# Kernel tuning notes

Measured on AMD Instinct MI355X. Metric: run time of the kernel, lower is better.

The kernel has to match this reference:

```python
import jax, jax.numpy as jnp
import numpy as np

B, H, S, D = 8, 8, 2048, 64

def setup_inputs() -> dict:
    key = jax.random.key(0)
    kq, kk, kv = jax.random.split(key, 3)
    queries = jax.random.normal(kq, (B, H, S, D), dtype=jnp.float32)
    keys = jax.random.normal(kk, (B, H, S, D), dtype=jnp.float32)
    values = jax.random.normal(kv, (B, H, S, D), dtype=jnp.float32)
    return {"queries": queries, "keys": keys, "values": values}

def reference(queries, keys, values):
    # scores: [B,H,S,S] = Q K^T / sqrt(D)
    scale = 1.0 / jnp.sqrt(jnp.asarray(queries.shape[-1], dtype=jnp.float32))
    scores = jnp.einsum('bhqd,bhkd->bhqk', queries, keys) * scale
    attn = jax.nn.softmax(scores, axis=-1)
    # dropout is identity at eval (p=0.0)
    return jnp.einsum('bhqk,bhkd->bhqd', attn, values)
```

## Files before the change

### kernel.cpp

```cpp
#include <hip/hip_runtime.h>

#define S_LEN 2048
#define HEAD_D 64
#define NH 64
#define KVB 64
#define NKT (S_LEN / KVB)
#define RS 72
#define KREG (KVB * RS)
#define IMG_USH (2 * KREG)
#define IMG_B (IMG_USH * 2)
#define WS_V5 ((size_t)NH * NKT * IMG_B)
#define IMG4_USH (KVB * HEAD_D * 2)

typedef float f32x4  __attribute__((ext_vector_type(4)));
typedef float f32x16 __attribute__((ext_vector_type(16)));
typedef __bf16 bf16x8 __attribute__((ext_vector_type(8)));

static __device__ __forceinline__ unsigned short f2bf(float x) {
  __bf16 h = (__bf16)x;
  return __builtin_bit_cast(unsigned short, h);
}
static __device__ __forceinline__ void gload_lds16(const void* g, void* l) {
  __builtin_amdgcn_global_load_lds(
      (const __attribute__((address_space(1))) unsigned int*)g,
      (__attribute__((address_space(3))) unsigned int*)l, 16, 0, 0);
}
static __device__ __forceinline__ int vpos(int kv) {
  return (kv & ~15) | (((kv >> 2) & 1) << 3) | (((kv >> 3) & 1) << 2) | (kv & 3);
}

__global__ __launch_bounds__(256) void pack_kv5(
    const float* __restrict__ K, const float* __restrict__ V,
    unsigned short* __restrict__ ws)
{
  const int kt = blockIdx.x;
  const int bh = blockIdx.y;
  const int t  = threadIdx.x;
  const float* Kg = K + ((size_t)bh * S_LEN + (size_t)kt * KVB) * HEAD_D;
  const float* Vg = V + ((size_t)bh * S_LEN + (size_t)kt * KVB) * HEAD_D;
  unsigned short* img = ws + ((size_t)bh * NKT + kt) * IMG_USH;

  __shared__ unsigned short vt[KREG];

#pragma unroll
  for (int i = 0; i < 4; ++i) {
    const int e   = t * 4 + i * 1024;
    const int row = e >> 6;
    const int col = e & 63;
    float4 k4 = *(const float4*)(Kg + e);
    ushort4 kb;
    kb.x = f2bf(k4.x); kb.y = f2bf(k4.y); kb.z = f2bf(k4.z); kb.w = f2bf(k4.w);
    *(ushort4*)&img[row * RS + col] = kb;
    float4 v4 = *(const float4*)(Vg + e);
    const int p = vpos(row);
    vt[(col + 0) * RS + p] = f2bf(v4.x);
    vt[(col + 1) * RS + p] = f2bf(v4.y);
    vt[(col + 2) * RS + p] = f2bf(v4.z);
    vt[(col + 3) * RS + p] = f2bf(v4.w);
  }
  __syncthreads();
  char* dst = (char*)(img + KREG);
  const char* src = (const char*)vt;
#pragma unroll
  for (int i = 0; i < 3; ++i) {
    const int off = t * 16 + i * 4096;
    if (off < 9216) *(uint4*)(dst + off) = *(const uint4*)(src + off);
  }
}

#define QBLK 256
#define NQT (S_LEN / QBLK)
__global__ __launch_bounds__(256, 2) void flash_attn_fwd_v6(
    const float* __restrict__ Q, const unsigned short* __restrict__ ws,
    float* __restrict__ O)
{
  __shared__ unsigned short lds[2][IMG_USH];

  const int tid  = threadIdx.x;
  const int wave = tid >> 6;
  const int lane = tid & 63;
  const int l31  = lane & 31;
  const int hi   = lane >> 5;

  const int bid = blockIdx.x;
  const int swz = (bid & 7) * 64 + (bid >> 3);
  const int bh  = swz >> 3;
  const int qt  = swz & 7;

  const float* Qh = Q + (size_t)bh * (S_LEN * HEAD_D);
  float*       Oh = O + (size_t)bh * (S_LEN * HEAD_D);
  const char*  gbase = (const char*)(ws + (size_t)bh * NKT * IMG_USH);

  const int qrowA = qt * QBLK + wave * 64 + l31;
  const int qrowB = qrowA + 32;

  bf16x8 qfA[4], qfB[4];
#pragma unroll
  for (int c = 0; c < 4; ++c) {
    const float* qa = Qh + (size_t)qrowA * HEAD_D + c * 16 + hi * 8;
    float4 a0 = *(const float4*)qa;
    float4 a1 = *(const float4*)(qa + 4);
    qfA[c][0] = (__bf16)a0.x; qfA[c][1] = (__bf16)a0.y;
    qfA[c][2] = (__bf16)a0.z; qfA[c][3] = (__bf16)a0.w;
    qfA[c][4] = (__bf16)a1.x; qfA[c][5] = (__bf16)a1.y;
    qfA[c][6] = (__bf16)a1.z; qfA[c][7] = (__bf16)a1.w;
    const float* qb = Qh + (size_t)qrowB * HEAD_D + c * 16 + hi * 8;
    float4 b0 = *(const float4*)qb;
    float4 b1 = *(const float4*)(qb + 4);
    qfB[c][0] = (__bf16)b0.x; qfB[c][1] = (__bf16)b0.y;
    qfB[c][2] = (__bf16)b0.z; qfB[c][3] = (__bf16)b0.w;
    qfB[c][4] = (__bf16)b1.x; qfB[c][5] = (__bf16)b1.y;
    qfB[c][6] = (__bf16)b1.z; qfB[c][7] = (__bf16)b1.w;
  }

  f32x16 oaA0, oaA1, oaB0, oaB1;
#pragma unroll
  for (int i = 0; i < 16; ++i) { oaA0[i] = 0.0f; oaA1[i] = 0.0f; oaB0[i] = 0.0f; oaB1[i] = 0.0f; }
  float lA = 0.0f, lB = 0.0f;
  const float K2 = 0.18033688f;
  const float C2 = -23.0831206f;

  auto stage = [&](const char* g, unsigned short* Lp) {
    char* lb = (char*)Lp;
#pragma unroll
    for (int i = 0; i < 5; ++i) {
      const int ch = wave + i * 4;
      if (ch < 18) gload_lds16(g + ch * 1024 + lane * 16, lb + ch * 1024);
    }
  };

  auto compute = [&](const unsigned short* Lp) {
    const char* ka = (const char*)Lp + l31 * 144 + hi * 16;
    f32x16 p0A, p1A, p0B, p1B;
#pragma unroll
    for (int i = 0; i < 16; ++i) { p0A[i] = 0.0f; p1A[i] = 0.0f; p0B[i] = 0.0f; p1B[i] = 0.0f; }
    __builtin_amdgcn_s_setprio(1);
#pragma unroll
    for (int c = 0; c < 4; ++c) {
      bf16x8 kf0 = *(const bf16x8*)(ka + c * 32);
      bf16x8 kf1 = *(const bf16x8*)(ka + 4608 + c * 32);
      p0A = __builtin_amdgcn_mfma_f32_32x32x16_bf16(kf0, qfA[c], p0A, 0, 0, 0);
      p0B = __builtin_amdgcn_mfma_f32_32x32x16_bf16(kf0, qfB[c], p0B, 0, 0, 0);
      p1A = __builtin_amdgcn_mfma_f32_32x32x16_bf16(kf1, qfA[c], p1A, 0, 0, 0);
      p1B = __builtin_amdgcn_mfma_f32_32x32x16_bf16(kf1, qfB[c], p1B, 0, 0, 0);
    }
    __builtin_amdgcn_s_setprio(0);

#pragma unroll
    for (int i = 0; i < 16; ++i) {
      p0A[i] = __builtin_amdgcn_exp2f(__builtin_fmaf(p0A[i], K2, C2));
      p1A[i] = __builtin_amdgcn_exp2f(__builtin_fmaf(p1A[i], K2, C2));
      p0B[i] = __builtin_amdgcn_exp2f(__builtin_fmaf(p0B[i], K2, C2));
      p1B[i] = __builtin_amdgcn_exp2f(__builtin_fmaf(p1B[i], K2, C2));
    }
    float sA[16], sB[16];
#pragma unroll
    for (int i = 0; i < 16; ++i) { sA[i] = p0A[i] + p1A[i]; sB[i] = p0B[i] + p1B[i]; }
#pragma unroll
    for (int st = 8; st >= 1; st >>= 1)
#pragma unroll
      for (int i = 0; i < st; ++i) { sA[i] += sA[i + st]; sB[i] += sB[i + st]; }
    lA += sA[0];
    lB += sB[0];

    __builtin_amdgcn_s_setprio(1);
#pragma unroll
    for (int kc = 0; kc < 4; ++kc) {
      const f32x16& psA = (kc < 2) ? p0A : p1A;
      const f32x16& psB = (kc < 2) ? p0B : p1B;
      const int rb = (kc & 1) * 8;
      unsigned a0, a1, a2, a3, b0, b1, b2, b3;
      asm("v_cvt_pk_bf16_f32 %0, %1, %2" : "=v"(a0) : "v"(psA[rb + 0]), "v"(psA[rb + 1]));
      asm("v_cvt_pk_bf16_f32 %0, %1, %2" : "=v"(a1) : "v"(psA[rb + 2]), "v"(psA[rb + 3]));
      asm("v_cvt_pk_bf16_f32 %0, %1, %2" : "=v"(a2) : "v"(psA[rb + 4]), "v"(psA[rb + 5]));
      asm("v_cvt_pk_bf16_f32 %0, %1, %2" : "=v"(a3) : "v"(psA[rb + 6]), "v"(psA[rb + 7]));
      asm("v_cvt_pk_bf16_f32 %0, %1, %2" : "=v"(b0) : "v"(psB[rb + 0]), "v"(psB[rb + 1]));
      asm("v_cvt_pk_bf16_f32 %0, %1, %2" : "=v"(b1) : "v"(psB[rb + 2]), "v"(psB[rb + 3]));
      asm("v_cvt_pk_bf16_f32 %0, %1, %2" : "=v"(b2) : "v"(psB[rb + 4]), "v"(psB[rb + 5]));
      asm("v_cvt_pk_bf16_f32 %0, %1, %2" : "=v"(b3) : "v"(psB[rb + 6]), "v"(psB[rb + 7]));
      uint4 wa; wa.x = a0; wa.y = a1; wa.z = a2; wa.w = a3;
      uint4 wb; wb.x = b0; wb.y = b1; wb.z = b2; wb.w = b3;
      bf16x8 pfA = __builtin_bit_cast(bf16x8, wa);
      bf16x8 pfB = __builtin_bit_cast(bf16x8, wb);
      bf16x8 vf0 = *(const bf16x8*)(ka + 9216 + kc * 32);
      bf16x8 vf1 = *(const bf16x8*)(ka + 9216 + 4608 + kc * 32);
      oaA0 = __builtin_amdgcn_mfma_f32_32x32x16_bf16(vf0, pfA, oaA0, 0, 0, 0);
      oaB0 = __builtin_amdgcn_mfma_f32_32x32x16_bf16(vf0, pfB, oaB0, 0, 0, 0);
      oaA1 = __builtin_amdgcn_mfma_f32_32x32x16_bf16(vf1, pfA, oaA1, 0, 0, 0);
      oaB1 = __builtin_amdgcn_mfma_f32_32x32x16_bf16(vf1, pfB, oaB1, 0, 0, 0);
    }
    __builtin_amdgcn_s_setprio(0);
  };

  stage(gbase, &lds[0][0]);
  __syncthreads();
  const char* g = gbase + IMG_B;

  for (int kt = 0; kt < NKT; kt += 2) {
    stage(g, &lds[1][0]);
    g += IMG_B;
    compute(&lds[0][0]);
    __syncthreads();
    const char* gs = (kt + 2 < NKT) ? g : gbase;
    stage(gs, &lds[0][0]);
    g += IMG_B;
    compute(&lds[1][0]);
    __syncthreads();
  }

  const float invA = 1.0f / (lA + __shfl_xor(lA, 32));
  const float invB = 1.0f / (lB + __shfl_xor(lB, 32));
  float* orA = Oh + (size_t)qrowA * HEAD_D;
  float* orB = Oh + (size_t)qrowB * HEAD_D;
#pragma unroll
  for (int gg = 0; gg < 4; ++gg) {
    float4 o;
    o.x = oaA0[4 * gg + 0] * invA; o.y = oaA0[4 * gg + 1] * invA;
    o.z = oaA0[4 * gg + 2] * invA; o.w = oaA0[4 * gg + 3] * invA;
    *(float4*)&orA[gg * 8 + hi * 4] = o;
    o.x = oaA1[4 * gg + 0] * invA; o.y = oaA1[4 * gg + 1] * invA;
    o.z = oaA1[4 * gg + 2] * invA; o.w = oaA1[4 * gg + 3] * invA;
    *(float4*)&orA[32 + gg * 8 + hi * 4] = o;
    o.x = oaB0[4 * gg + 0] * invB; o.y = oaB0[4 * gg + 1] * invB;
    o.z = oaB0[4 * gg + 2] * invB; o.w = oaB0[4 * gg + 3] * invB;
    *(float4*)&orB[gg * 8 + hi * 4] = o;
    o.x = oaB1[4 * gg + 0] * invB; o.y = oaB1[4 * gg + 1] * invB;
    o.z = oaB1[4 * gg + 2] * invB; o.w = oaB1[4 * gg + 3] * invB;
    *(float4*)&orB[32 + gg * 8 + hi * 4] = o;
  }
}

__global__ __launch_bounds__(256) void pack_kv4(
    const float* __restrict__ K, const float* __restrict__ V,
    unsigned short* __restrict__ ws)
{
  const int kt = blockIdx.x;
  const int bh = blockIdx.y;
  const int t  = threadIdx.x;
  const float* Kg = K + ((size_t)bh * S_LEN + (size_t)kt * KVB) * HEAD_D;
  const float* Vg = V + ((size_t)bh * S_LEN + (size_t)kt * KVB) * HEAD_D;
  unsigned short* img = ws + ((size_t)bh * NKT + kt) * IMG4_USH;
  __shared__ unsigned short vt[HEAD_D * KVB];
#pragma unroll
  for (int i = 0; i < 4; ++i) {
    const int e   = t * 4 + i * 1024;
    const int row = e >> 6;
    const int col = e & 63;
    float4 k4 = *(const float4*)(Kg + e);
    ushort4 kb;
    kb.x = f2bf(k4.x); kb.y = f2bf(k4.y); kb.z = f2bf(k4.z); kb.w = f2bf(k4.w);
    *(ushort4*)&img[row * 64 + (col ^ ((row & 7) << 3))] = kb;
    float4 v4 = *(const float4*)(Vg + e);
    const int p = vpos(row);
    vt[(col + 0) * 64 + (p ^ (((col + 0) & 7) << 3))] = f2bf(v4.x);
    vt[(col + 1) * 64 + (p ^ (((col + 1) & 7) << 3))] = f2bf(v4.y);
    vt[(col + 2) * 64 + (p ^ (((col + 2) & 7) << 3))] = f2bf(v4.z);
    vt[(col + 3) * 64 + (p ^ (((col + 3) & 7) << 3))] = f2bf(v4.w);
  }
  __syncthreads();
  uint4* dst = (uint4*)(img + KVB * HEAD_D);
  const uint4* src = (const uint4*)vt;
#pragma unroll
  for (int i = 0; i < 2; ++i) dst[t + i * 256] = src[t + i * 256];
}

__global__ __launch_bounds__(256, 2) void flash_attn_fwd_v4(
    const float* __restrict__ Q, const unsigned short* __restrict__ ws,
    float* __restrict__ O)
{
  __shared__ unsigned short lds[2][IMG4_USH];
  const int tid  = threadIdx.x;
  const int wave = tid >> 6;
  const int lane = tid & 63;
  const int l31  = lane & 31;
  const int hi   = lane >> 5;
  const int bid = blockIdx.x;
  const int swz = (bid & 7) * 128 + (bid >> 3);
  const int bh  = swz >> 4;
  const int qt  = swz & 15;
  const float* Qh = Q + (size_t)bh * (S_LEN * HEAD_D);
  float*       Oh = O + (size_t)bh * (S_LEN * HEAD_D);
  const unsigned short* imgh = ws + (size_t)bh * NKT * IMG4_USH;
  const int qrow = qt * 128 + wave * 32 + l31;
  bf16x8 qf[4];
#pragma unroll
  for (int c = 0; c < 4; ++c) {
    const float* qp = Qh + (size_t)qrow * HEAD_D + c * 16 + hi * 8;
    float4 a = *(const float4*)qp;
    float4 b = *(const float4*)(qp + 4);
    qf[c][0] = (__bf16)a.x; qf[c][1] = (__bf16)a.y;
    qf[c][2] = (__bf16)a.z; qf[c][3] = (__bf16)a.w;
    qf[c][4] = (__bf16)b.x; qf[c][5] = (__bf16)b.y;
    qf[c][6] = (__bf16)b.z; qf[c][7] = (__bf16)b.w;
  }
  f32x16 oa0, oa1;
#pragma unroll
  for (int i = 0; i < 16; ++i) { oa0[i] = 0.0f; oa1[i] = 0.0f; }
  float m_run = -1e30f, l_run = 0.0f;
  const float SC = 0.125f;
  {
    const char* gg = (const char*)imgh;
    char* l = (char*)&lds[0][0];
    const int wb = wave * 4096;
#pragma unroll
    for (int c2 = 0; c2 < 4; ++c2) {
      const int off = wb + c2 * 1024;
      gload_lds16(gg + off + lane * 16, l + off);
    }
  }
  __syncthreads();
  int cur = 0;
  for (int kt = 0; kt < NKT; ++kt) {
    if (kt + 1 < NKT) {
      const char* gg = (const char*)(imgh + (size_t)(kt + 1) * IMG4_USH);
      char* l = (char*)&lds[cur ^ 1][0];
      const int wb = wave * 4096;
#pragma unroll
      for (int c2 = 0; c2 < 4; ++c2) {
        const int off = wb + c2 * 1024;
        gload_lds16(gg + off + lane * 16, l + off);
      }
    }
    const unsigned short* kT = &lds[cur][0];
    const unsigned short* vT = &lds[cur][KVB * HEAD_D];
    f32x16 p0, p1;
#pragma unroll
    for (int i = 0; i < 16; ++i) { p0[i] = 0.0f; p1[i] = 0.0f; }
    __builtin_amdgcn_s_setprio(1);
#pragma unroll
    for (int c = 0; c < 4; ++c) {
      const int r0 = l31;
      bf16x8 kf0 = *(const bf16x8*)&kT[r0 * 64 + ((c * 16 + hi * 8) ^ ((r0 & 7) << 3))];
      p0 = __builtin_amdgcn_mfma_f32_32x32x16_bf16(kf0, qf[c], p0, 0, 0, 0);
      const int r1 = l31 + 32;
      bf16x8 kf1 = *(const bf16x8*)&kT[r1 * 64 + ((c * 16 + hi * 8) ^ ((r1 & 7) << 3))];
      p1 = __builtin_amdgcn_mfma_f32_32x32x16_bf16(kf1, qf[c], p1, 0, 0, 0);
    }
    __builtin_amdgcn_s_setprio(0);
    float t16[16];
#pragma unroll
    for (int i = 0; i < 16; ++i) t16[i] = fmaxf(p0[i], p1[i]);
#pragma unroll
    for (int st = 8; st >= 1; st >>= 1)
#pragma unroll
      for (int i = 0; i < st; ++i) t16[i] = fmaxf(t16[i], t16[i + st]);
    const float tmax = fmaxf(t16[0], __shfl_xor(t16[0], 32));
    const int defer = __all((tmax - m_run) <= 64.0f);
    if (!defer) {
      const float mnew = fmaxf(m_run, tmax);
      const float corr = __expf((m_run - mnew) * SC);
      m_run = mnew;
      l_run *= corr;
#pragma unroll
      for (int i = 0; i < 16; ++i) { oa0[i] *= corr; oa1[i] *= corr; }
    }
    const float msc = m_run * SC;
#pragma unroll
    for (int i = 0; i < 16; ++i) {
      p0[i] = __expf(__builtin_fmaf(p0[i], SC, -msc));
      p1[i] = __expf(__builtin_fmaf(p1[i], SC, -msc));
    }
    float s16[16];
#pragma unroll
    for (int i = 0; i < 16; ++i) s16[i] = p0[i] + p1[i];
#pragma unroll
    for (int st = 8; st >= 1; st >>= 1)
#pragma unroll
      for (int i = 0; i < st; ++i) s16[i] = s16[i] + s16[i + st];
    l_run += s16[0] + __shfl_xor(s16[0], 32);
    __builtin_amdgcn_s_setprio(1);
#pragma unroll
    for (int kc = 0; kc < 4; ++kc) {
      const f32x16& ps = (kc < 2) ? p0 : p1;
      const int rb = (kc & 1) * 8;
      uint4 wv;
      wv.x = (unsigned)f2bf(ps[rb + 0]) | ((unsigned)f2bf(ps[rb + 1]) << 16);
      wv.y = (unsigned)f2bf(ps[rb + 2]) | ((unsigned)f2bf(ps[rb + 3]) << 16);
      wv.z = (unsigned)f2bf(ps[rb + 4]) | ((unsigned)f2bf(ps[rb + 5]) << 16);
      wv.w = (unsigned)f2bf(ps[rb + 6]) | ((unsigned)f2bf(ps[rb + 7]) << 16);
      bf16x8 pf = __builtin_bit_cast(bf16x8, wv);
#pragma unroll
      for (int db = 0; db < 2; ++db) {
        const int d = db * 32 + l31;
        bf16x8 vf = *(const bf16x8*)&vT[d * 64 + ((kc * 16 + hi * 8) ^ ((d & 7) << 3))];
        if (db == 0) oa0 = __builtin_amdgcn_mfma_f32_32x32x16_bf16(vf, pf, oa0, 0, 0, 0);
        else         oa1 = __builtin_amdgcn_mfma_f32_32x32x16_bf16(vf, pf, oa1, 0, 0, 0);
      }
    }
    __builtin_amdgcn_s_setprio(0);
    __syncthreads();
    cur ^= 1;
  }
  const float inv = 1.0f / l_run;
  float* orow = Oh + (size_t)qrow * HEAD_D;
#pragma unroll
  for (int gg = 0; gg < 4; ++gg) {
    float4 o4;
    o4.x = oa0[4 * gg + 0] * inv; o4.y = oa0[4 * gg + 1] * inv;
    o4.z = oa0[4 * gg + 2] * inv; o4.w = oa0[4 * gg + 3] * inv;
    *(float4*)&orow[gg * 8 + hi * 4] = o4;
    float4 o5;
    o5.x = oa1[4 * gg + 0] * inv; o5.y = oa1[4 * gg + 1] * inv;
    o5.z = oa1[4 * gg + 2] * inv; o5.w = oa1[4 * gg + 3] * inv;
    *(float4*)&orow[32 + gg * 8 + hi * 4] = o5;
  }
}

extern "C" void kernel_launch(void* const* d_in, const int* in_sizes, int n_in,
                              void* d_out, int out_size, void* d_ws, size_t ws_size,
                              hipStream_t stream) {
  const float* Q = (const float*)d_in[0];
  const float* K = (const float*)d_in[1];
  const float* V = (const float*)d_in[2];
  float* O = (float*)d_out;
  unsigned short* ws = (unsigned short*)d_ws;
  if (ws_size >= WS_V5) {
    hipLaunchKernelGGL(pack_kv5, dim3(NKT, NH), dim3(256), 0, stream, K, V, ws);
    hipLaunchKernelGGL(flash_attn_fwd_v6, dim3(512), dim3(256), 0, stream, Q, ws, O);
  } else {
    hipLaunchKernelGGL(pack_kv4, dim3(NKT, NH), dim3(256), 0, stream, K, V, ws);
    hipLaunchKernelGGL(flash_attn_fwd_v4, dim3(1024), dim3(256), 0, stream, Q, ws, O);
  }
}
```

Measured before the change: 100.8 us.

## Fold softmax scale into Q, compute row sums via MFMA, stage two KV tiles ahead

Q is pre-multiplied by the log2e/sqrt(D) factor so the per-score FMA before exp2 goes away. The constant offset C2 is dropped, which is safe only while no exponent overflows. The per-lane row-sum reduction is replaced by extra MFMAs against a ones matrix, moving VALU adds onto the matrix unit. LDS is doubled to four buffers so two tiles are staged while two are computed, with one barrier per pair instead of two. This raises LDS use, which may limit the two-blocks-per-CU occupancy, and adds MFMA work and accumulator registers.

Measured after the change: 101.4 us. About the same (+0.6%).

```diff
diff --git a/kernel.cpp b/kernel.cpp
--- a/kernel.cpp
+++ b/kernel.cpp
@@ -69,12 +69,11 @@
 }
 
 #define QBLK 256
-#define NQT (S_LEN / QBLK)
-__global__ __launch_bounds__(256, 2) void flash_attn_fwd_v6(
+__global__ __launch_bounds__(256, 2) void flash_attn_fwd_v7(
     const float* __restrict__ Q, const unsigned short* __restrict__ ws,
     float* __restrict__ O)
 {
-  __shared__ unsigned short lds[2][IMG_USH];
+  __shared__ unsigned short lds[4][IMG_USH];
 
   const int tid  = threadIdx.x;
   const int wave = tid >> 6;
@@ -94,31 +93,36 @@
   const int qrowA = qt * QBLK + wave * 64 + l31;
   const int qrowB = qrowA + 32;
 
+  const float K2 = 0.18033688f;
   bf16x8 qfA[4], qfB[4];
 #pragma unroll
   for (int c = 0; c < 4; ++c) {
     const float* qa = Qh + (size_t)qrowA * HEAD_D + c * 16 + hi * 8;
     float4 a0 = *(const float4*)qa;
     float4 a1 = *(const float4*)(qa + 4);
-    qfA[c][0] = (__bf16)a0.x; qfA[c][1] = (__bf16)a0.y;
-    qfA[c][2] = (__bf16)a0.z; qfA[c][3] = (__bf16)a0.w;
-    qfA[c][4] = (__bf16)a1.x; qfA[c][5] = (__bf16)a1.y;
-    qfA[c][6] = (__bf16)a1.z; qfA[c][7] = (__bf16)a1.w;
+    qfA[c][0] = (__bf16)(a0.x * K2); qfA[c][1] = (__bf16)(a0.y * K2);
+    qfA[c][2] = (__bf16)(a0.z * K2); qfA[c][3] = (__bf16)(a0.w * K2);
+    qfA[c][4] = (__bf16)(a1.x * K2); qfA[c][5] = (__bf16)(a1.y * K2);
+    qfA[c][6] = (__bf16)(a1.z * K2); qfA[c][7] = (__bf16)(a1.w * K2);
     const float* qb = Qh + (size_t)qrowB * HEAD_D + c * 16 + hi * 8;
     float4 b0 = *(const float4*)qb;
     float4 b1 = *(const float4*)(qb + 4);
-    qfB[c][0] = (__bf16)b0.x; qfB[c][1] = (__bf16)b0.y;
-    qfB[c][2] = (__bf16)b0.z; qfB[c][3] = (__bf16)b0.w;
-    qfB[c][4] = (__bf16)b1.x; qfB[c][5] = (__bf16)b1.y;
-    qfB[c][6] = (__bf16)b1.z; qfB[c][7] = (__bf16)b1.w;
-  }
-
-  f32x16 oaA0, oaA1, oaB0, oaB1;
-#pragma unroll
-  for (int i = 0; i < 16; ++i) { oaA0[i] = 0.0f; oaA1[i] = 0.0f; oaB0[i] = 0.0f; oaB1[i] = 0.0f; }
-  float lA = 0.0f, lB = 0.0f;
-  const float K2 = 0.18033688f;
-  const float C2 = -23.0831206f;
+    qfB[c][0] = (__bf16)(b0.x * K2); qfB[c][1] = (__bf16)(b0.y * K2);
+    qfB[c][2] = (__bf16)(b0.z * K2); qfB[c][3] = (__bf16)(b0.w * K2);
+    qfB[c][4] = (__bf16)(b1.x * K2); qfB[c][5] = (__bf16)(b1.y * K2);
+    qfB[c][6] = (__bf16)(b1.z * K2); qfB[c][7] = (__bf16)(b1.w * K2);
+  }
+
+  bf16x8 onef;
+#pragma unroll
+  for (int i = 0; i < 8; ++i) onef[i] = (__bf16)1.0f;
+
+  f32x16 oaA0, oaA1, oaB0, oaB1, oaLA, oaLB;
+#pragma unroll
+  for (int i = 0; i < 16; ++i) {
+    oaA0[i] = 0.0f; oaA1[i] = 0.0f; oaB0[i] = 0.0f; oaB1[i] = 0.0f;
+    oaLA[i] = 0.0f; oaLB[i] = 0.0f;
+  }
 
   auto stage = [&](const char* g, unsigned short* Lp) {
     char* lb = (char*)Lp;
@@ -148,20 +152,11 @@
 
 #pragma unroll
     for (int i = 0; i < 16; ++i) {
-      p0A[i] = __builtin_amdgcn_exp2f(__builtin_fmaf(p0A[i], K2, C2));
-      p1A[i] = __builtin_amdgcn_exp2f(__builtin_fmaf(p1A[i], K2, C2));
-      p0B[i] = __builtin_amdgcn_exp2f(__builtin_fmaf(p0B[i], K2, C2));
-      p1B[i] = __builtin_amdgcn_exp2f(__builtin_fmaf(p1B[i], K2, C2));
-    }
-    float sA[16], sB[16];
-#pragma unroll
-    for (int i = 0; i < 16; ++i) { sA[i] = p0A[i] + p1A[i]; sB[i] = p0B[i] + p1B[i]; }
-#pragma unroll
-    for (int st = 8; st >= 1; st >>= 1)
-#pragma unroll
-      for (int i = 0; i < st; ++i) { sA[i] += sA[i + st]; sB[i] += sB[i + st]; }
-    lA += sA[0];
-    lB += sB[0];
+      p0A[i] = __builtin_amdgcn_exp2f(p0A[i]);
+      p1A[i] = __builtin_amdgcn_exp2f(p1A[i]);
+      p0B[i] = __builtin_amdgcn_exp2f(p0B[i]);
+      p1B[i] = __builtin_amdgcn_exp2f(p1B[i]);
+    }
 
     __builtin_amdgcn_s_setprio(1);
 #pragma unroll
@@ -188,28 +183,30 @@
       oaB0 = __builtin_amdgcn_mfma_f32_32x32x16_bf16(vf0, pfB, oaB0, 0, 0, 0);
       oaA1 = __builtin_amdgcn_mfma_f32_32x32x16_bf16(vf1, pfA, oaA1, 0, 0, 0);
       oaB1 = __builtin_amdgcn_mfma_f32_32x32x16_bf16(vf1, pfB, oaB1, 0, 0, 0);
+      oaLA = __builtin_amdgcn_mfma_f32_32x32x16_bf16(onef, pfA, oaLA, 0, 0, 0);
+      oaLB = __builtin_amdgcn_mfma_f32_32x32x16_bf16(onef, pfB, oaLB, 0, 0, 0);
     }
     __builtin_amdgcn_s_setprio(0);
   };
 
   stage(gbase, &lds[0][0]);
+  stage(gbase + IMG_B, &lds[1][0]);
   __syncthreads();
-  const char* g = gbase + IMG_B;
 
   for (int kt = 0; kt < NKT; kt += 2) {
-    stage(g, &lds[1][0]);
-    g += IMG_B;
-    compute(&lds[0][0]);
+    const int cb = (kt & 2) ? 2 : 0;
+    const int sb = cb ^ 2;
+    const char* g2 = (kt + 2 < NKT) ? gbase + (size_t)(kt + 2) * IMG_B : gbase;
+    const char* g3 = (kt + 3 < NKT) ? gbase + (size_t)(kt + 3) * IMG_B : gbase;
+    stage(g2, &lds[sb][0]);
+    stage(g3, &lds[sb + 1][0]);
+    compute(&lds[cb][0]);
+    compute(&lds[cb + 1][0]);
     __syncthreads();
-    const char* gs = (kt + 2 < NKT) ? g : gbase;
-    stage(gs, &lds[0][0]);
-    g += IMG_B;
-    compute(&lds[1][0]);
-    __syncthreads();
-  }
-
-  const float invA = 1.0f / (lA + __shfl_xor(lA, 32));
-  const float invB = 1.0f / (lB + __shfl_xor(lB, 32));
+  }
+
+  const float invA = 1.0f / oaLA[0];
+  const float invB = 1.0f / oaLB[0];
   float* orA = Oh + (size_t)qrowA * HEAD_D;
   float* orB = Oh + (size_t)qrowB * HEAD_D;
 #pragma unroll
@@ -416,7 +413,7 @@
   unsigned short* ws = (unsigned short*)d_ws;
   if (ws_size >= WS_V5) {
     hipLaunchKernelGGL(pack_kv5, dim3(NKT, NH), dim3(256), 0, stream, K, V, ws);
-    hipLaunchKernelGGL(flash_attn_fwd_v6, dim3(512), dim3(256), 0, stream, Q, ws, O);
+    hipLaunchKernelGGL(flash_attn_fwd_v7, dim3(512), dim3(256), 0, stream, Q, ws, O);
   } else {
     hipLaunchKernelGGL(pack_kv4, dim3(NKT, NH), dim3(256), 0, stream, K, V, ws);
     hipLaunchKernelGGL(flash_attn_fwd_v4, dim3(1024), dim3(256), 0, stream, Q, ws, O);
```
